# Optimization experiments

Hardware: AMD Instinct MI355X
Metric: run time of the kernel (lower is better)

The kernel has to match this reference:

```python
import jax, jax.numpy as jnp
import numpy as np
from jax import lax


def _mdlstm_dir(x, Wx, Wh, Wv, b):
    # x: [H, W, B, Cin]; one diagonal-causal 2D-LSTM scan (top-left origin).
    H, W, B, Cin = x.shape
    C = Wh.shape[0]
    xa = jnp.einsum('hwbi,ic->hwbc', x, Wx) + b  # [H,W,B,5C] precomputed input gates

    def col_step(carry, inp):
        h_l, c_l = carry                    # left neighbor [B,C]
        xa_ij, h_u, c_u = inp               # input preact, up neighbor
        a = xa_ij + h_l @ Wh + h_u @ Wv     # [B,5C]
        i, f1, f2, o, g = jnp.split(a, 5, axis=-1)
        c = jax.nn.sigmoid(i) * jnp.tanh(g) + jax.nn.sigmoid(f1) * c_l + jax.nn.sigmoid(f2) * c_u
        h = jax.nn.sigmoid(o) * jnp.tanh(c)
        return (h, c), (h, c)

    z = jnp.zeros((B, C), x.dtype)
    zrow = jnp.zeros((W, B, C), x.dtype)

    def row_step(carry, xa_row):
        h_up, c_up = carry                  # [W,B,C]
        _, (hs, cs) = lax.scan(col_step, (z, z), (xa_row, h_up, c_up))
        return (hs, cs), hs

    _, hh = lax.scan(row_step, (zrow, zrow), xa)  # [H,W,B,C]
    return hh


def _mdlstm4(x, Wx, Wh, Wv, b):
    # x: [B,Cin,H,W] -> per-direction outputs [4,H,W,B,C] (directions: TL, TR, BL, BR origins)
    xt = jnp.transpose(x, (2, 3, 0, 1))  # [H,W,B,Cin]
    x4 = jnp.stack([xt, xt[:, ::-1], xt[::-1], xt[::-1, ::-1]])
    o = jax.vmap(_mdlstm_dir)(x4, Wx, Wh, Wv, b)  # [4,H,W,B,C]
    return jnp.stack([o[0], o[1][:, ::-1], o[2][::-1], o[3][::-1, ::-1]])


def _block(x, Wx, Wh, Wv, b, cw, cb):
    h4 = _mdlstm4(x, Wx, Wh, Wv, b)            # [4,H,W,B,C]
    h = jnp.transpose(h4.sum(0), (2, 3, 0, 1))  # sum directions -> [B,C,H,W]
    y = lax.conv_general_dilated(h, cw, window_strides=(2, 2), padding='VALID',
                                 dimension_numbers=('NCHW', 'OIHW', 'NCHW'))
    return jnp.tanh(y + cb[None, :, None, None])


def _forward(x, p0_Wx, p0_Wh, p0_Wv, p0_b, c0_w, c0_b,
             p1_Wx, p1_Wh, p1_Wv, p1_b, c1_w, c1_b,
             p2_Wx, p2_Wh, p2_Wv, p2_b, dW, db):
    x = _block(x, p0_Wx, p0_Wh, p0_Wv, p0_b, c0_w, c0_b)  # [B,6,31,126]
    x = _block(x, p1_Wx, p1_Wh, p1_Wv, p1_b, c1_w, c1_b)  # [B,20,14,61]
    h4 = _mdlstm4(x, p2_Wx, p2_Wh, p2_Wv, p2_b)           # [4,H,W,B,50]
    # per-direction Linear(50->100) then sum over the 4 directions
    out = jnp.einsum('dhwbc,dcn->bhwn', h4, dW) + db.sum(0)
    return out  # [B,14,61,100]


def setup_inputs() -> dict:
    key = jax.random.key(0)
    ks = jax.random.split(key, 20)
    rn = lambda k, s, sc=0.1: jax.random.normal(k, s, jnp.float32) * sc
    return {
        'x': jax.random.normal(ks[0], (16, 1, 64, 256), jnp.float32),
        'p0_Wx': rn(ks[1], (4, 1, 10)), 'p0_Wh': rn(ks[2], (4, 2, 10)),
        'p0_Wv': rn(ks[3], (4, 2, 10)), 'p0_b': rn(ks[4], (4, 10)),
        'c0_w': rn(ks[5], (6, 2, 2, 4)), 'c0_b': rn(ks[6], (6,)),
        'p1_Wx': rn(ks[7], (4, 6, 50)), 'p1_Wh': rn(ks[8], (4, 10, 50)),
        'p1_Wv': rn(ks[9], (4, 10, 50)), 'p1_b': rn(ks[10], (4, 50)),
        'c1_w': rn(ks[11], (20, 10, 2, 4)), 'c1_b': rn(ks[12], (20,)),
        'p2_Wx': rn(ks[13], (4, 20, 250)), 'p2_Wh': rn(ks[14], (4, 50, 250)),
        'p2_Wv': rn(ks[15], (4, 50, 250)), 'p2_b': rn(ks[16], (4, 250)),
        'dW': rn(ks[17], (4, 50, 100)), 'db': rn(ks[18], (4, 100)),
    }


def reference(x, p0_Wx, p0_Wh, p0_Wv, p0_b, c0_w, c0_b,
              p1_Wx, p1_Wh, p1_Wv, p1_b, c1_w, c1_b,
              p2_Wx, p2_Wh, p2_Wv, p2_b, dW, db):
    return _forward(x, p0_Wx, p0_Wh, p0_Wv, p0_b, c0_w, c0_b,
                    p1_Wx, p1_Wh, p1_Wv, p1_b, c1_w, c1_b,
                    p2_Wx, p2_Wh, p2_Wv, p2_b, dW, db)
```

## Files before the change

### kernel.cpp

```cpp
#include <hip/hip_runtime.h>

typedef unsigned short ushort_t;
typedef __attribute__((ext_vector_type(8))) short short8;
typedef __attribute__((ext_vector_type(4))) float float4_t;
typedef __attribute__((ext_vector_type(2))) float v2f;

__device__ __forceinline__ float frcp(float x) { return __builtin_amdgcn_rcpf(x); }
__device__ __forceinline__ float fsig(float x) { return frcp(1.f + __expf(-x)); }
__device__ __forceinline__ float ftanh(float x) { return 1.f - 2.f * frcp(1.f + __expf(2.f * x)); }
__device__ __forceinline__ float sig_e2(float a) { return frcp(1.f + __builtin_amdgcn_exp2f(a)); }
__device__ __forceinline__ float th_e2(float a) { return 1.f - 2.f * frcp(1.f + __builtin_amdgcn_exp2f(a)); }

__device__ __forceinline__ float exp2_fma(float a) {
    a = fminf(fmaxf(a, -60.f), 60.f);
    float k = floorf(a);
    float f = a - k;
    float p = fmaf(f, 1.54035304e-4f, 1.33335581e-3f);
    p = fmaf(f, p, 9.61812911e-3f);
    p = fmaf(f, p, 5.55041087e-2f);
    p = fmaf(f, p, 2.40226507e-1f);
    p = fmaf(f, p, 6.93147181e-1f);
    p = fmaf(f, p, 1.0f);
    int ik = (int)k;
    float sc = __builtin_bit_cast(float, (ik + 127) << 23);
    return p * sc;
}
__device__ __forceinline__ float rcp_fma(float y) {
    int i = 0x7EF311C3 - __builtin_bit_cast(int, y);
    float r = __builtin_bit_cast(float, i);
    r = r * fmaf(-y, r, 2.0f);
    r = r * fmaf(-y, r, 2.0f);
    return r;
}
__device__ __forceinline__ float sig_e2f(float a) { return rcp_fma(1.f + exp2_fma(a)); }
__device__ __forceinline__ float th_e2f(float a)  { return fmaf(-2.f, rcp_fma(1.f + exp2_fma(a)), 1.f); }

__device__ __forceinline__ ushort_t f2bf(float f) {
    union { float f; unsigned u; } v; v.f = f;
    unsigned u = v.u;
    unsigned r = (u + 0x7fffu + ((u >> 16) & 1u)) >> 16;
    return (ushort_t)r;
}
__device__ __forceinline__ float bf2f(ushort_t s) {
    union { unsigned u; float f; } v; v.u = ((unsigned)s) << 16;
    return v.f;
}
__device__ __forceinline__ float dpp_shr1(float x) {
    int i = __builtin_bit_cast(int, x);
    int r = __builtin_amdgcn_update_dpp(0, i, 0x138 , 0xf, 0xf, true);
    return __builtin_bit_cast(float, r);
}

__global__ __launch_bounds__(64) void k_mdlstm0(
    const float* __restrict__ x, const float* __restrict__ Wx,
    const float* __restrict__ Wh, const float* __restrict__ Wv,
    const float* __restrict__ bias, float* __restrict__ h0)
{
    const int dir = blockIdx.x >> 4, b = blockIdx.x & 15;
    const int lane = threadIdx.x;
    const bool fH = dir >= 2, fW = (dir & 1) != 0;
    const int ri = fH ? 63 - lane : lane;
    const float L2E = 1.44269504088896340736f;

    __shared__ float Xs[64 * 256];
    {
        const float* xg = x + b * 64 * 256;
        for (int i4 = lane; i4 < 4096; i4 += 64) {
            int row = i4 >> 6, c4 = (i4 & 63) << 2;
            float4 v = *(const float4*)(xg + (row << 8) + c4);
            *(float4*)&Xs[(row << 8) + c4] = v;
        }
    }
    __syncthreads();

    v2f wx[5], bs[5], wh0[5], wh1[5], wv0[5], wv1[5];
#pragma unroll
    for (int g = 0; g < 5; g++) {
        float sc = (g == 4) ? 2.f * L2E : -L2E;
#pragma unroll
        for (int un = 0; un < 2; un++) {
            int n = g * 2 + un;
            wx[g][un]  = Wx[dir * 10 + n] * sc;
            bs[g][un]  = bias[dir * 10 + n] * sc;
            wh0[g][un] = Wh[(dir * 2 + 0) * 10 + n] * sc;
            wh1[g][un] = Wh[(dir * 2 + 1) * 10 + n] * sc;
            wv0[g][un] = Wv[(dir * 2 + 0) * 10 + n] * sc;
            wv1[g][un] = Wv[(dir * 2 + 1) * 10 + n] * sc;
        }
    }

    float* orow = h0 + (((dir * 16 + b) * 64 + ri) * 256) * 2;
    v2f hB = {0.f, 0.f}, cB = {0.f, 0.f};

    auto ldx = [&](int j) -> float {
        int jc = j < 0 ? 0 : (j > 255 ? 255 : j);
        int cj = fW ? 255 - jc : jc;
        return Xs[(ri << 8) + cj];
    };
    auto cellf = [&](float xv, v2f hl, v2f cl, float hu0, float hu1,
                     float cu0, float cu1, v2f& hn, v2f& cn) {
        v2f a[5];
#pragma unroll
        for (int g = 0; g < 5; g++) {
            v2f t = __builtin_elementwise_fma((v2f){xv, xv}, wx[g], bs[g]);
            t = __builtin_elementwise_fma((v2f){hl.x, hl.x}, wh0[g], t);
            t = __builtin_elementwise_fma((v2f){hl.y, hl.y}, wh1[g], t);
            t = __builtin_elementwise_fma((v2f){hu0, hu0}, wv0[g], t);
            t = __builtin_elementwise_fma((v2f){hu1, hu1}, wv1[g], t);
            a[g] = t;
        }
        v2f si  = {sig_e2f(a[0].x), sig_e2f(a[0].y)};
        v2f sf1 = {sig_e2f(a[1].x), sig_e2f(a[1].y)};
        v2f sf2 = {sig_e2f(a[2].x), sig_e2f(a[2].y)};
        v2f so  = {sig_e2f(a[3].x), sig_e2f(a[3].y)};
        v2f tg  = {th_e2f(a[4].x),  th_e2f(a[4].y)};
        v2f cu  = {cu0, cu1};
        cn = si * tg + sf1 * cl + sf2 * cu;
        v2f tc = {th_e2f(cn.x * (2.f * L2E)), th_e2f(cn.y * (2.f * L2E))};
        hn = so * tc;
    };

    float xA0 = ldx(0 - lane), xB0 = ldx(1 - lane);
    float xA1 = ldx(2 - lane), xB1 = ldx(3 - lane);

    for (int t = 0; t < 160; t++) {
        const int jA = 2 * t - lane, jB = jA + 1;
        float xA = xA0, xB = xB0;
        xA0 = xA1; xB0 = xB1;
        xA1 = ldx(2 * (t + 2) - lane); xB1 = ldx(2 * (t + 2) + 1 - lane);

        float huA0 = dpp_shr1(hB.x), huA1 = dpp_shr1(hB.y);
        float cuA0 = dpp_shr1(cB.x), cuA1 = dpp_shr1(cB.y);
        v2f hA, cA;
        cellf(xA, hB, cB, huA0, huA1, cuA0, cuA1, hA, cA);
        bool actA = (jA >= 0) && (jA < 256);
        if (!actA) { hA = (v2f){0.f, 0.f}; cA = (v2f){0.f, 0.f}; }

        float huB0 = dpp_shr1(hA.x), huB1 = dpp_shr1(hA.y);
        float cuB0 = dpp_shr1(cA.x), cuB1 = dpp_shr1(cA.y);
        v2f hN, cN;
        cellf(xB, hA, cA, huB0, huB1, cuB0, cuB1, hN, cN);
        bool actB = (jB >= 0) && (jB < 256);
        if (!actB) { hN = (v2f){0.f, 0.f}; cN = (v2f){0.f, 0.f}; }
        hB = hN; cB = cN;

        if (actA) {
            int cj = fW ? 255 - jA : jA;
            float2 hv; hv.x = hA.x; hv.y = hA.y;
            *(float2*)&orow[cj * 2] = hv;
        }
        if (actB) {
            int cj = fW ? 255 - jB : jB;
            float2 hv; hv.x = hB.x; hv.y = hB.y;
            *(float2*)&orow[cj * 2] = hv;
        }
    }
}

__global__ __launch_bounds__(128) void k_conv0(
    const float* __restrict__ h0, const float* __restrict__ cw,
    const float* __restrict__ cb, float* __restrict__ x1)
{
    int blk = blockIdx.x;
    int oh = blk / 127, ow = blk % 127;
    int t = threadIdx.x;
    if (t >= 96) return;
    int b = t / 6, co = t % 6;
    float w[2][2][4];
#pragma unroll
    for (int ci = 0; ci < 2; ci++)
#pragma unroll
        for (int kh = 0; kh < 2; kh++)
#pragma unroll
            for (int kw = 0; kw < 4; kw++)
                w[ci][kh][kw] = cw[((co * 2 + ci) * 2 + kh) * 4 + kw];
    float acc = cb[co];
    for (int dirb = 0; dirb < 4; dirb++) {
#pragma unroll
        for (int kh = 0; kh < 2; kh++) {
#pragma unroll
            for (int kw = 0; kw < 4; kw++) {
                const float* ptr = h0 + ((((dirb * 16 + b) * 64) + (2 * oh + kh)) * 256 + (2 * ow + kw)) * 2;
                float2 hv = *(const float2*)ptr;
                acc = fmaf(hv.x, w[0][kh][kw], acc);
                acc = fmaf(hv.y, w[1][kh][kw], acc);
            }
        }
    }
    x1[((oh * 127 + ow) * 16 + b) * 6 + co] = ftanh(acc);
}

__global__ __launch_bounds__(1024, 1) void k_mdlstm1(
    const float* __restrict__ x1, const float* __restrict__ Wx,
    const float* __restrict__ Wh, const float* __restrict__ Wv,
    const float* __restrict__ bias, float* __restrict__ h1)
{
    const int dir = blockIdx.x >> 4, b = blockIdx.x & 15;
    const bool fH = dir >= 2, fW = (dir & 1) != 0;
    const int tid = threadIdx.x;
    const int wave = tid >> 6, lane = tid & 63;

    __shared__ float Xs1[32 * 127 * 6];
    __shared__ __align__(16) ushort_t Ah[2][32][40];
    __shared__ __align__(16) ushort_t Al[2][32][40];
    __shared__ float P[32][68];
    __shared__ float cbuf[2][33][12];

    for (int i = tid; i < 2 * 32 * 40; i += 1024) { ((ushort_t*)Ah)[i] = 0; ((ushort_t*)Al)[i] = 0; }
    for (int i = tid; i < 2 * 33 * 12; i += 1024) ((float*)cbuf)[i] = 0.f;
    for (int i = tid; i < 32 * 127 * 6; i += 1024)
        Xs1[i] = x1[(i / 6) * 96 + b * 6 + (i % 6)];
    __syncthreads();
    if (tid < 6) {
        int rr = fH ? 31 : 0, cc = fW ? 126 : 0;
        float xv = Xs1[(rr * 127 + cc) * 6 + tid];
        ushort_t xh = f2bf(xv);
        Ah[0][0][20 + tid] = xh;
        Al[0][0][20 + tid] = f2bf(xv - bf2f(xh));
    }

    const int mt = wave & 1, nt = wave >> 1;
    short8 bh = {0,0,0,0,0,0,0,0}, bl = {0,0,0,0,0,0,0,0};
    if (wave < 8) {
        int n = nt * 16 + (lane & 15);
#pragma unroll
        for (int jj = 0; jj < 8; jj++) {
            int k = (lane >> 4) * 8 + jj;
            float v = 0.f;
            if (n < 50) {
                if (k < 10)      v = Wh[(dir * 10 + k) * 50 + n];
                else if (k < 20) v = Wv[(dir * 10 + (k - 10)) * 50 + n];
                else if (k < 26) v = Wx[(dir * 6 + (k - 20)) * 50 + n];
            }
            ushort_t hi = f2bf(v);
            bh[jj] = (short)hi;
            bl[jj] = (short)f2bf(v - bf2f(hi));
        }
    }

    const int cell = tid / 10, u = tid % 10;
    float br[5];
#pragma unroll
    for (int g = 0; g < 5; g++) br[g] = (tid < 320) ? bias[dir * 50 + g * 10 + u] : 0.f;
    const int ri = fH ? 31 - cell : cell;
    float creg = 0.f;
    __syncthreads();

    int p = 0;
    for (int d = 0; d < 158; d++) {
        if (wave < 8) {
            const int arow = mt * 16 + (lane & 15);
            const int koff = (lane >> 4) * 8;
            short8 ah = *(const short8*)&Ah[p][arow][koff];
            short8 al = *(const short8*)&Al[p][arow][koff];
            float4_t acc = {0.f, 0.f, 0.f, 0.f};
            acc = __builtin_amdgcn_mfma_f32_16x16x32_bf16(ah, bh, acc, 0, 0, 0);
            acc = __builtin_amdgcn_mfma_f32_16x16x32_bf16(al, bh, acc, 0, 0, 0);
            acc = __builtin_amdgcn_mfma_f32_16x16x32_bf16(ah, bl, acc, 0, 0, 0);
            int col = nt * 16 + (lane & 15);
            int r0 = (lane >> 4) * 4;
#pragma unroll
            for (int r = 0; r < 4; r++) P[mt * 16 + r0 + r][col] = acc[r];
        } else if (tid >= 512 && tid < 704) {
            int s = tid - 512, xc = s / 6, ci = s % 6;
            int jn = d + 1 - xc;
            if (jn >= 0 && jn < 127) {
                int rr = fH ? 31 - xc : xc, cc = fW ? 126 - jn : jn;
                float xv = Xs1[(rr * 127 + cc) * 6 + ci];
                ushort_t xh = f2bf(xv);
                Ah[1 - p][xc][20 + ci] = xh;
                Al[1 - p][xc][20 + ci] = f2bf(xv - bf2f(xh));
            }
        }
        __syncthreads();

        if (tid < 320) {
            int j = d - cell;
            if (j >= 0 && j < 127) {
                float ai  = P[cell][u]      + br[0];
                float af1 = P[cell][10 + u] + br[1];
                float af2 = P[cell][20 + u] + br[2];
                float ao  = P[cell][30 + u] + br[3];
                float ag  = P[cell][40 + u] + br[4];
                float cu = cbuf[p][cell][u];
                float cn = fsig(ai) * ftanh(ag) + fsig(af1) * creg + fsig(af2) * cu;
                float hn = fsig(ao) * ftanh(cn);
                creg = cn;
                cbuf[1 - p][cell + 1][u] = cn;
                ushort_t hh = f2bf(hn);
                float hhf = bf2f(hh);
                ushort_t hlo = f2bf(hn - hhf);
                Ah[1 - p][cell][u] = hh;
                Al[1 - p][cell][u] = hlo;
                if (cell < 31) { Ah[1 - p][cell + 1][10 + u] = hh; Al[1 - p][cell + 1][10 + u] = hlo; }
                int cj = fW ? 126 - j : j;
                h1[(((dir * 16 + b) * 32 + ri) * 127 + cj) * 10 + u] = hn;
            }
        }
        __syncthreads();
        p ^= 1;
    }
}

__global__ __launch_bounds__(320, 1) void k_conv1(
    const float* __restrict__ h1, const float* __restrict__ cw,
    const float* __restrict__ cb, float* __restrict__ x2)
{
    int blk = blockIdx.x;
    int oh = blk / 62, ow = blk % 62;
    int t = threadIdx.x;
    int b = t / 20, co = t % 20;
    float w[10][2][4];
#pragma unroll
    for (int ci = 0; ci < 10; ci++)
#pragma unroll
        for (int kh = 0; kh < 2; kh++)
#pragma unroll
            for (int kw = 0; kw < 4; kw++)
                w[ci][kh][kw] = cw[((co * 10 + ci) * 2 + kh) * 4 + kw];
    float acc = cb[co];
    for (int dirb = 0; dirb < 4; dirb++) {
#pragma unroll
        for (int kh = 0; kh < 2; kh++) {
#pragma unroll
            for (int kw = 0; kw < 4; kw++) {
                const float* ptr = h1 + ((((dirb * 16 + b) * 32) + (2 * oh + kh)) * 127 + (2 * ow + kw)) * 10;
#pragma unroll
                for (int ci = 0; ci < 10; ci++)
                    acc = fmaf(ptr[ci], w[ci][kh][kw], acc);
            }
        }
    }
    x2[((oh * 62 + ow) * 16 + b) * 20 + co] = ftanh(acc);
}

__global__ __launch_bounds__(256) void k_prepB2(
    const float* __restrict__ Wh, const float* __restrict__ Wv,
    const float* __restrict__ Wx, ushort_t* __restrict__ Bh,
    ushort_t* __restrict__ Bl)
{
    int idx = blockIdx.x * 256 + threadIdx.x;
    if (idx >= 131072) return;
    int dir = idx >> 15; int k = (idx >> 8) & 127; int n = idx & 255;
    float v = 0.f;
    if (n < 250) {
        if (k < 50)       v = Wh[(dir * 50 + k) * 250 + n];
        else if (k < 100) v = Wv[(dir * 50 + (k - 50)) * 250 + n];
        else if (k < 120) v = Wx[(dir * 20 + (k - 100)) * 250 + n];
    }
    ushort_t hi = f2bf(v);
    Bh[idx] = hi;
    Bl[idx] = f2bf(v - bf2f(hi));
}

__global__ __launch_bounds__(1024, 1) void k_mdlstm2(
    const float* __restrict__ x2, const ushort_t* __restrict__ BmH,
    const ushort_t* __restrict__ BmL,
    const float* __restrict__ bias, float* __restrict__ h2)
{
    const int dir = blockIdx.x >> 4, b = blockIdx.x & 15;
    const bool fH = dir >= 2, fW = (dir & 1) != 0;
    const int tid = threadIdx.x;
    const int wave = tid >> 6, lane = tid & 63;

    __shared__ float Xs2[16 * 62 * 20];
    __shared__ __align__(16) ushort_t Ah[2][16][136];
    __shared__ __align__(16) ushort_t Al[2][16][136];
    __shared__ float P[16][260];
    __shared__ float cbuf[2][16][52];

    for (int i = tid; i < 2 * 16 * 136; i += 1024) { ((ushort_t*)Ah)[i] = 0; ((ushort_t*)Al)[i] = 0; }
    for (int i = tid; i < 16 * 62 * 20; i += 1024)
        Xs2[i] = x2[(i / 20) * 320 + b * 20 + (i % 20)];
    __syncthreads();
    if (tid < 20) {
        int ci = tid;
        int rr = fH ? 15 : 0, cc = fW ? 61 : 0;
        float xv = Xs2[(rr * 62 + cc) * 20 + ci];
        ushort_t xh = f2bf(xv);
        Ah[0][0][100 + ci] = xh;
        Al[0][0][100 + ci] = f2bf(xv - bf2f(xh));
    }

    short8 bfragH[4], bfragL[4];
    {
        const int n = wave * 16 + (lane & 15);
#pragma unroll
        for (int q = 0; q < 4; q++) {
#pragma unroll
            for (int jj = 0; jj < 8; jj++) {
                int k = q * 32 + (lane >> 4) * 8 + jj;
                bfragH[q][jj] = (short)BmH[(dir * 128 + k) * 256 + n];
                bfragL[q][jj] = (short)BmL[(dir * 128 + k) * 256 + n];
            }
        }
    }

    const int cell = tid / 50, u = tid % 50;
    float bi = 0, bf1 = 0, bf2v = 0, bo = 0, bg = 0;
    if (tid < 800) {
        bi   = bias[dir * 250 + u];
        bf1  = bias[dir * 250 + 50 + u];
        bf2v = bias[dir * 250 + 100 + u];
        bo   = bias[dir * 250 + 150 + u];
        bg   = bias[dir * 250 + 200 + u];
    }
    const int rr_c = fH ? 15 - cell : cell;
    float creg = 0.f;
    __syncthreads();

    int p = 0;
    for (int d = 0; d < 77; d++) {
        {
            const int arow = lane & 15;
            const int koff = (lane >> 4) * 8;
            short8 ah[4], al[4];
#pragma unroll
            for (int q = 0; q < 4; q++) {
                ah[q] = *(const short8*)&Ah[p][arow][q * 32 + koff];
                al[q] = *(const short8*)&Al[p][arow][q * 32 + koff];
            }
            float4_t acc = {0.f, 0.f, 0.f, 0.f};
#pragma unroll
            for (int q = 0; q < 4; q++) acc = __builtin_amdgcn_mfma_f32_16x16x32_bf16(ah[q], bfragH[q], acc, 0, 0, 0);
#pragma unroll
            for (int q = 0; q < 4; q++) acc = __builtin_amdgcn_mfma_f32_16x16x32_bf16(al[q], bfragH[q], acc, 0, 0, 0);
#pragma unroll
            for (int q = 0; q < 4; q++) acc = __builtin_amdgcn_mfma_f32_16x16x32_bf16(ah[q], bfragL[q], acc, 0, 0, 0);
            int col = wave * 16 + (lane & 15);
            int r0 = (lane >> 4) * 4;
#pragma unroll
            for (int r = 0; r < 4; r++) P[r0 + r][col] = acc[r];
        }
        __syncthreads();

        if (tid < 800) {
            int j = d - cell;
            if (j >= 0 && j < 62) {
                float ai  = P[cell][u] + bi;
                float af1 = P[cell][50 + u] + bf1;
                float af2 = P[cell][100 + u] + bf2v;
                float ao  = P[cell][150 + u] + bo;
                float ag  = P[cell][200 + u] + bg;
                float cu = (cell == 0) ? 0.f : cbuf[p][cell - 1][u];
                float cn = fsig(ai) * ftanh(ag) + fsig(af1) * creg + fsig(af2) * cu;
                float hn = fsig(ao) * ftanh(cn);
                creg = cn;
                cbuf[1 - p][cell][u] = cn;
                ushort_t hh = f2bf(hn);
                float hhf = bf2f(hh);
                ushort_t hlo = f2bf(hn - hhf);
                Ah[1 - p][cell][u] = hh;
                Al[1 - p][cell][u] = hlo;
                if (cell < 15) { Ah[1 - p][cell + 1][50 + u] = hh; Al[1 - p][cell + 1][50 + u] = hlo; }
                int cc = fW ? 61 - j : j;
                h2[(((dir * 16 + b) * 16 + rr_c) * 62 + cc) * 50 + u] = hn;
            }
        } else if (tid >= 832 && tid < 992) {
            int s = tid - 832;
#pragma unroll
            for (int it = 0; it < 2; it++) {
                int item = s + it * 160;
                int xc = item / 20, ci = item % 20;
                int jn = d + 1 - xc;
                if (jn >= 0 && jn < 62) {
                    int rr = fH ? 15 - xc : xc, cc = fW ? 61 - jn : jn;
                    float xv = Xs2[(rr * 62 + cc) * 20 + ci];
                    ushort_t xh = f2bf(xv);
                    Ah[1 - p][xc][100 + ci] = xh;
                    Al[1 - p][xc][100 + ci] = f2bf(xv - bf2f(xh));
                }
            }
        }
        __syncthreads();
        p ^= 1;
    }
}

__global__ __launch_bounds__(256) void k_final(
    const float* __restrict__ h2, const float* __restrict__ dW,
    const float* __restrict__ db, float* __restrict__ out)
{
    int blk = blockIdx.x;
    int r = blk / 62, c = blk % 62;
    int t = threadIdx.x;
    __shared__ float hb[3200];
    for (int i = t; i < 3200; i += 256) {
        int dirb = i / 800, rem = i % 800, b = rem / 50, u = rem % 50;
        hb[i] = h2[(((dirb * 16 + b) * 16 + r) * 62 + c) * 50 + u];
    }
    __syncthreads();
    for (int o = t; o < 1600; o += 256) {
        int b = o / 100, n = o % 100;
        float acc = db[n] + db[100 + n] + db[200 + n] + db[300 + n];
#pragma unroll
        for (int dirb = 0; dirb < 4; dirb++) {
            const float* hp = hb + (dirb * 16 + b) * 50;
            const float* wp = dW + dirb * 5000 + n;
#pragma unroll 10
            for (int cc2 = 0; cc2 < 50; cc2++)
                acc = fmaf(hp[cc2], wp[cc2 * 100], acc);
        }
        out[((b * 16 + r) * 62 + c) * 100 + n] = acc;
    }
}

extern "C" void kernel_launch(void* const* d_in, const int* in_sizes, int n_in,
                              void* d_out, int out_size, void* d_ws, size_t ws_size,
                              hipStream_t stream)
{
    const float* x     = (const float*)d_in[0];
    const float* p0_Wx = (const float*)d_in[1];
    const float* p0_Wh = (const float*)d_in[2];
    const float* p0_Wv = (const float*)d_in[3];
    const float* p0_b  = (const float*)d_in[4];
    const float* c0_w  = (const float*)d_in[5];
    const float* c0_b  = (const float*)d_in[6];
    const float* p1_Wx = (const float*)d_in[7];
    const float* p1_Wh = (const float*)d_in[8];
    const float* p1_Wv = (const float*)d_in[9];
    const float* p1_b  = (const float*)d_in[10];
    const float* c1_w  = (const float*)d_in[11];
    const float* c1_b  = (const float*)d_in[12];
    const float* p2_Wx = (const float*)d_in[13];
    const float* p2_Wh = (const float*)d_in[14];
    const float* p2_Wv = (const float*)d_in[15];
    const float* p2_b  = (const float*)d_in[16];
    const float* dW    = (const float*)d_in[17];
    const float* db    = (const float*)d_in[18];
    float* out = (float*)d_out;
    float* ws  = (float*)d_ws;

    float* h0 = ws;
    float* x1 = h0 + 2097152;
    float* h1 = x1 + 390144;
    float* x2 = h1 + 2600960;
    float* h2 = x2 + 317440;
    ushort_t* BmH = (ushort_t*)(h2 + 3174400);
    ushort_t* BmL = BmH + 131072;

    k_prepB2<<<512, 256, 0, stream>>>(p2_Wh, p2_Wv, p2_Wx, BmH, BmL);
    k_mdlstm0<<<64, 64, 0, stream>>>(x, p0_Wx, p0_Wh, p0_Wv, p0_b, h0);
    k_conv0<<<32 * 127, 128, 0, stream>>>(h0, c0_w, c0_b, x1);
    k_mdlstm1<<<64, 1024, 0, stream>>>(x1, p1_Wx, p1_Wh, p1_Wv, p1_b, h1);
    k_conv1<<<16 * 62, 320, 0, stream>>>(h1, c1_w, c1_b, x2);
    k_mdlstm2<<<64, 1024, 0, stream>>>(x2, BmH, BmL, p2_b, h2);
    k_final<<<16 * 62, 256, 0, stream>>>(h2, dW, db, out);
}
```

Measured before the change: 538.4 us.

## Shrink mdlstm1 blocks to 320 threads and use hardware exp2/rcp in mdlstm0

k_mdlstm1 drops from 1024 to 320 threads per block. Each of its 4 MFMA waves now computes two 16-column N tiles, and the fifth wave stages the x inputs in three passes. The smaller block is meant to lower the cost of the per-diagonal __syncthreads and remove idle waves. k_mdlstm0 replaces its FMA-polynomial exp2 and reciprocal approximations with the hardware exp2 and rcp instructions, cutting ALU work per cell at the cost of transcendental-unit throughput and slightly different numerics.

```diff
diff --git a/kernel.cpp b/kernel.cpp
--- a/kernel.cpp
+++ b/kernel.cpp
@@ -10,30 +10,6 @@
 __device__ __forceinline__ float ftanh(float x) { return 1.f - 2.f * frcp(1.f + __expf(2.f * x)); }
 __device__ __forceinline__ float sig_e2(float a) { return frcp(1.f + __builtin_amdgcn_exp2f(a)); }
 __device__ __forceinline__ float th_e2(float a) { return 1.f - 2.f * frcp(1.f + __builtin_amdgcn_exp2f(a)); }
-
-__device__ __forceinline__ float exp2_fma(float a) {
-    a = fminf(fmaxf(a, -60.f), 60.f);
-    float k = floorf(a);
-    float f = a - k;
-    float p = fmaf(f, 1.54035304e-4f, 1.33335581e-3f);
-    p = fmaf(f, p, 9.61812911e-3f);
-    p = fmaf(f, p, 5.55041087e-2f);
-    p = fmaf(f, p, 2.40226507e-1f);
-    p = fmaf(f, p, 6.93147181e-1f);
-    p = fmaf(f, p, 1.0f);
-    int ik = (int)k;
-    float sc = __builtin_bit_cast(float, (ik + 127) << 23);
-    return p * sc;
-}
-__device__ __forceinline__ float rcp_fma(float y) {
-    int i = 0x7EF311C3 - __builtin_bit_cast(int, y);
-    float r = __builtin_bit_cast(float, i);
-    r = r * fmaf(-y, r, 2.0f);
-    r = r * fmaf(-y, r, 2.0f);
-    return r;
-}
-__device__ __forceinline__ float sig_e2f(float a) { return rcp_fma(1.f + exp2_fma(a)); }
-__device__ __forceinline__ float th_e2f(float a)  { return fmaf(-2.f, rcp_fma(1.f + exp2_fma(a)), 1.f); }
 
 __device__ __forceinline__ ushort_t f2bf(float f) {
     union { float f; unsigned u; } v; v.f = f;
@@ -109,14 +85,14 @@
             t = __builtin_elementwise_fma((v2f){hu1, hu1}, wv1[g], t);
             a[g] = t;
         }
-        v2f si  = {sig_e2f(a[0].x), sig_e2f(a[0].y)};
-        v2f sf1 = {sig_e2f(a[1].x), sig_e2f(a[1].y)};
-        v2f sf2 = {sig_e2f(a[2].x), sig_e2f(a[2].y)};
-        v2f so  = {sig_e2f(a[3].x), sig_e2f(a[3].y)};
-        v2f tg  = {th_e2f(a[4].x),  th_e2f(a[4].y)};
+        v2f si  = {sig_e2(a[0].x), sig_e2(a[0].y)};
+        v2f sf1 = {sig_e2(a[1].x), sig_e2(a[1].y)};
+        v2f sf2 = {sig_e2(a[2].x), sig_e2(a[2].y)};
+        v2f so  = {sig_e2(a[3].x), sig_e2(a[3].y)};
+        v2f tg  = {th_e2(a[4].x),  th_e2(a[4].y)};
         v2f cu  = {cu0, cu1};
         cn = si * tg + sf1 * cl + sf2 * cu;
-        v2f tc = {th_e2f(cn.x * (2.f * L2E)), th_e2f(cn.y * (2.f * L2E))};
+        v2f tc = {th_e2(cn.x * (2.f * L2E)), th_e2(cn.y * (2.f * L2E))};
         hn = so * tc;
     };
 
@@ -190,7 +166,7 @@
     x1[((oh * 127 + ow) * 16 + b) * 6 + co] = ftanh(acc);
 }
 
-__global__ __launch_bounds__(1024, 1) void k_mdlstm1(
+__global__ __launch_bounds__(320, 1) void k_mdlstm1(
     const float* __restrict__ x1, const float* __restrict__ Wx,
     const float* __restrict__ Wh, const float* __restrict__ Wv,
     const float* __restrict__ bias, float* __restrict__ h1)
@@ -206,9 +182,9 @@
     __shared__ float P[32][68];
     __shared__ float cbuf[2][33][12];
 
-    for (int i = tid; i < 2 * 32 * 40; i += 1024) { ((ushort_t*)Ah)[i] = 0; ((ushort_t*)Al)[i] = 0; }
-    for (int i = tid; i < 2 * 33 * 12; i += 1024) ((float*)cbuf)[i] = 0.f;
-    for (int i = tid; i < 32 * 127 * 6; i += 1024)
+    for (int i = tid; i < 2 * 32 * 40; i += 320) { ((ushort_t*)Ah)[i] = 0; ((ushort_t*)Al)[i] = 0; }
+    for (int i = tid; i < 2 * 33 * 12; i += 320) ((float*)cbuf)[i] = 0.f;
+    for (int i = tid; i < 32 * 127 * 6; i += 320)
         Xs1[i] = x1[(i / 6) * 96 + b * 6 + (i % 6)];
     __syncthreads();
     if (tid < 6) {
@@ -219,62 +195,77 @@
         Al[0][0][20 + tid] = f2bf(xv - bf2f(xh));
     }
 
-    const int mt = wave & 1, nt = wave >> 1;
-    short8 bh = {0,0,0,0,0,0,0,0}, bl = {0,0,0,0,0,0,0,0};
-    if (wave < 8) {
-        int n = nt * 16 + (lane & 15);
-#pragma unroll
-        for (int jj = 0; jj < 8; jj++) {
-            int k = (lane >> 4) * 8 + jj;
-            float v = 0.f;
-            if (n < 50) {
-                if (k < 10)      v = Wh[(dir * 10 + k) * 50 + n];
-                else if (k < 20) v = Wv[(dir * 10 + (k - 10)) * 50 + n];
-                else if (k < 26) v = Wx[(dir * 6 + (k - 20)) * 50 + n];
-            }
-            ushort_t hi = f2bf(v);
-            bh[jj] = (short)hi;
-            bl[jj] = (short)f2bf(v - bf2f(hi));
+    const int mt = wave & 1, nt0 = (wave >> 1) * 2;
+    short8 bh0 = {0,0,0,0,0,0,0,0}, bl0 = {0,0,0,0,0,0,0,0};
+    short8 bh1 = {0,0,0,0,0,0,0,0}, bl1 = {0,0,0,0,0,0,0,0};
+    if (wave < 4) {
+#pragma unroll
+        for (int t = 0; t < 2; t++) {
+            int n = (nt0 + t) * 16 + (lane & 15);
+#pragma unroll
+            for (int jj = 0; jj < 8; jj++) {
+                int k = (lane >> 4) * 8 + jj;
+                float v = 0.f;
+                if (n < 50) {
+                    if (k < 10)      v = Wh[(dir * 10 + k) * 50 + n];
+                    else if (k < 20) v = Wv[(dir * 10 + (k - 10)) * 50 + n];
+                    else if (k < 26) v = Wx[(dir * 6 + (k - 20)) * 50 + n];
+                }
+                ushort_t hi = f2bf(v);
+                ushort_t lo = f2bf(v - bf2f(hi));
+                if (t == 0) { bh0[jj] = (short)hi; bl0[jj] = (short)lo; }
+                else        { bh1[jj] = (short)hi; bl1[jj] = (short)lo; }
+            }
         }
     }
 
     const int cell = tid / 10, u = tid % 10;
     float br[5];
 #pragma unroll
-    for (int g = 0; g < 5; g++) br[g] = (tid < 320) ? bias[dir * 50 + g * 10 + u] : 0.f;
+    for (int g = 0; g < 5; g++) br[g] = bias[dir * 50 + g * 10 + u];
     const int ri = fH ? 31 - cell : cell;
     float creg = 0.f;
     __syncthreads();
 
     int p = 0;
     for (int d = 0; d < 158; d++) {
-        if (wave < 8) {
+        if (wave < 4) {
             const int arow = mt * 16 + (lane & 15);
             const int koff = (lane >> 4) * 8;
             short8 ah = *(const short8*)&Ah[p][arow][koff];
             short8 al = *(const short8*)&Al[p][arow][koff];
-            float4_t acc = {0.f, 0.f, 0.f, 0.f};
-            acc = __builtin_amdgcn_mfma_f32_16x16x32_bf16(ah, bh, acc, 0, 0, 0);
-            acc = __builtin_amdgcn_mfma_f32_16x16x32_bf16(al, bh, acc, 0, 0, 0);
-            acc = __builtin_amdgcn_mfma_f32_16x16x32_bf16(ah, bl, acc, 0, 0, 0);
-            int col = nt * 16 + (lane & 15);
+            float4_t acc0 = {0.f, 0.f, 0.f, 0.f};
+            float4_t acc1 = {0.f, 0.f, 0.f, 0.f};
+            acc0 = __builtin_amdgcn_mfma_f32_16x16x32_bf16(ah, bh0, acc0, 0, 0, 0);
+            acc1 = __builtin_amdgcn_mfma_f32_16x16x32_bf16(ah, bh1, acc1, 0, 0, 0);
+            acc0 = __builtin_amdgcn_mfma_f32_16x16x32_bf16(al, bh0, acc0, 0, 0, 0);
+            acc1 = __builtin_amdgcn_mfma_f32_16x16x32_bf16(al, bh1, acc1, 0, 0, 0);
+            acc0 = __builtin_amdgcn_mfma_f32_16x16x32_bf16(ah, bl0, acc0, 0, 0, 0);
+            acc1 = __builtin_amdgcn_mfma_f32_16x16x32_bf16(ah, bl1, acc1, 0, 0, 0);
+            int col0 = nt0 * 16 + (lane & 15);
             int r0 = (lane >> 4) * 4;
 #pragma unroll
-            for (int r = 0; r < 4; r++) P[mt * 16 + r0 + r][col] = acc[r];
-        } else if (tid >= 512 && tid < 704) {
-            int s = tid - 512, xc = s / 6, ci = s % 6;
-            int jn = d + 1 - xc;
-            if (jn >= 0 && jn < 127) {
-                int rr = fH ? 31 - xc : xc, cc = fW ? 126 - jn : jn;
-                float xv = Xs1[(rr * 127 + cc) * 6 + ci];
-                ushort_t xh = f2bf(xv);
-                Ah[1 - p][xc][20 + ci] = xh;
-                Al[1 - p][xc][20 + ci] = f2bf(xv - bf2f(xh));
+            for (int r = 0; r < 4; r++) P[mt * 16 + r0 + r][col0] = acc0[r];
+#pragma unroll
+            for (int r = 0; r < 4; r++) P[mt * 16 + r0 + r][col0 + 16] = acc1[r];
+        } else {
+#pragma unroll
+            for (int it = 0; it < 3; it++) {
+                int item = lane + it * 64;
+                int xc = item / 6, ci = item % 6;
+                int jn = d + 1 - xc;
+                if (jn >= 0 && jn < 127) {
+                    int rr = fH ? 31 - xc : xc, cc = fW ? 126 - jn : jn;
+                    float xv = Xs1[(rr * 127 + cc) * 6 + ci];
+                    ushort_t xh = f2bf(xv);
+                    Ah[1 - p][xc][20 + ci] = xh;
+                    Al[1 - p][xc][20 + ci] = f2bf(xv - bf2f(xh));
+                }
             }
         }
         __syncthreads();
 
-        if (tid < 320) {
+        {
             int j = d - cell;
             if (j >= 0 && j < 127) {
                 float ai  = P[cell][u]      + br[0];
@@ -542,7 +533,7 @@
     k_prepB2<<<512, 256, 0, stream>>>(p2_Wh, p2_Wv, p2_Wx, BmH, BmL);
     k_mdlstm0<<<64, 64, 0, stream>>>(x, p0_Wx, p0_Wh, p0_Wv, p0_b, h0);
     k_conv0<<<32 * 127, 128, 0, stream>>>(h0, c0_w, c0_b, x1);
-    k_mdlstm1<<<64, 1024, 0, stream>>>(x1, p1_Wx, p1_Wh, p1_Wv, p1_b, h1);
+    k_mdlstm1<<<64, 320, 0, stream>>>(x1, p1_Wx, p1_Wh, p1_Wv, p1_b, h1);
     k_conv1<<<16 * 62, 320, 0, stream>>>(h1, c1_w, c1_b, x2);
     k_mdlstm2<<<64, 1024, 0, stream>>>(x2, BmH, BmL, p2_b, h2);
     k_final<<<16 * 62, 256, 0, stream>>>(h2, dW, db, out);
```

Result: faster. 494.2 us (-8.2%).
